# Kernel tuning notes

Hardware: AMD Instinct MI355X
Metric: run time of the kernel (lower is better)

## Reference

```python
import jax, jax.numpy as jnp
import numpy as np

B, T, C = 2, 2048, 1024
H = 16
D = C // H  # head_dim = 64


def setup_inputs() -> dict:
    key = jax.random.key(0)
    k1, k2, k3 = jax.random.split(key, 3)
    x = jax.random.normal(k1, (B, T, C), dtype=jnp.float32)
    # causal mask: True means 'mask out' (masked_fill semantics)
    attn_mask = jnp.triu(jnp.ones((T, T), dtype=bool), k=1)[None, None]
    W_attn = jax.random.normal(k2, (C, 3 * C), dtype=jnp.float32) * (1.0 / np.sqrt(C))
    b_attn = jnp.zeros((3 * C,), dtype=jnp.float32)
    W_proj = jax.random.normal(k3, (C, C), dtype=jnp.float32) * (1.0 / np.sqrt(C))
    b_proj = jnp.zeros((C,), dtype=jnp.float32)
    return {"x": x, "attn_mask": attn_mask, "W_attn": W_attn, "b_attn": b_attn,
            "W_proj": W_proj, "b_proj": b_proj}


def reference(x, attn_mask, W_attn, b_attn, W_proj, b_proj):
    Bb, Tt, Cc = x.shape
    qkv = x @ W_attn + b_attn                      # [B,T,3C]
    q, k, v = jnp.split(qkv, 3, axis=-1)
    def to_heads(t):
        return t.reshape(Bb, Tt, H, D).transpose(0, 2, 1, 3)  # [B,H,T,D]
    q, k, v = to_heads(q), to_heads(k), to_heads(v)
    scale = 1.0 / np.sqrt(D).astype(np.float32)
    attn = jnp.einsum('bhqd,bhkd->bhqk', q, k) * scale  # [B,H,T,T]
    attn = jnp.where(attn_mask, -jnp.inf, attn)
    attn = jax.nn.softmax(attn, axis=-1)
    y = jnp.einsum('bhqk,bhkd->bhqd', attn, v)          # [B,H,T,D]
    y = y.transpose(0, 2, 1, 3).reshape(Bb, Tt, Cc)
    return y @ W_proj + b_proj
```

## Files before the change

kernel.cpp:

```cpp
#include <hip/hip_runtime.h>
#include <math.h>


#define TSEQ 2048
#define NHD  16
#define DH   64
#define CDIM 1024

typedef __attribute__((ext_vector_type(8))) short bf16x8;
typedef __attribute__((ext_vector_type(4))) float f32x4;

#define MFMA(a, b, c) __builtin_amdgcn_mfma_f32_16x16x32_bf16((a), (b), (c), 0, 0, 0)

__device__ __forceinline__ ushort f2bf(float f) {
    unsigned u = __builtin_bit_cast(unsigned, f);
    u += 0x7FFFu + ((u >> 16) & 1u);
    return (ushort)(u >> 16);
}
__device__ __forceinline__ float bf2f(ushort h) {
    unsigned u = ((unsigned)h) << 16;
    return __builtin_bit_cast(float, u);
}

__global__ __launch_bounds__(256) void cast_k(const float* __restrict__ in,
                                              ushort* __restrict__ out, int n4) {
    int i = blockIdx.x * 256 + threadIdx.x;
    const int stride = gridDim.x * 256;
    for (; i < n4; i += stride) {
        float4 f = ((const float4*)in)[i];
        ushort4 o;
        o.x = f2bf(f.x); o.y = f2bf(f.y); o.z = f2bf(f.z); o.w = f2bf(f.w);
        ((ushort4*)out)[i] = o;
    }
}

__global__ __launch_bounds__(256) void transpose_k(const float* __restrict__ in,
                                                   ushort* __restrict__ out,
                                                   int R, int C) {
    __shared__ float t[32][33];
    const int tx = threadIdx.x, ty = threadIdx.y;
    const int c0 = blockIdx.x * 32, r0 = blockIdx.y * 32;
#pragma unroll
    for (int i = 0; i < 4; ++i)
        t[ty + i * 8][tx] = in[(size_t)(r0 + ty + i * 8) * C + c0 + tx];
    __syncthreads();
#pragma unroll
    for (int i = 0; i < 4; ++i)
        out[(size_t)(c0 + ty + i * 8) * R + r0 + tx] = f2bf(t[tx][ty + i * 8]);
}

__global__ __launch_bounds__(256) void qkv_k(const ushort* __restrict__ X,
                                             const ushort* __restrict__ Wt,
                                             const float* __restrict__ bias,
                                             ushort* __restrict__ qb,
                                             ushort* __restrict__ kb,
                                             ushort* __restrict__ vtb) {
    const int fid = blockIdx.x;
    const int nf = (fid & 7) * 96 + (fid >> 3);
    const int mt = nf / 24, nt = nf % 24;
    const int m0 = mt * 128, n0 = nt * 128;
    const int tid = threadIdx.x, lane = tid & 63, w = tid >> 6;
    const int l15 = lane & 15, g = lane >> 4;
    const int wm = w >> 1, wn = w & 1;

    const ushort* Ar[4]; const ushort* Br[4];
#pragma unroll
    for (int s = 0; s < 4; ++s) {
        Ar[s] = X  + (size_t)(m0 + wm * 64 + s * 16 + l15) * 1024 + g * 8;
        Br[s] = Wt + (size_t)(n0 + wn * 64 + s * 16 + l15) * 1024 + g * 8;
    }
    f32x4 acc[4][4] = {};
    bf16x8 a[4], b[4], a2[4], b2[4];
#pragma unroll
    for (int s = 0; s < 4; ++s) { a[s] = *(const bf16x8*)(Ar[s]); b[s] = *(const bf16x8*)(Br[s]); }

    for (int kk = 0; kk < 1024; kk += 32) {
        if (kk + 32 < 1024) {
#pragma unroll
            for (int s = 0; s < 4; ++s) {
                a2[s] = *(const bf16x8*)(Ar[s] + kk + 32);
                b2[s] = *(const bf16x8*)(Br[s] + kk + 32);
            }
        }
#pragma unroll
        for (int i = 0; i < 4; ++i)
#pragma unroll
            for (int j = 0; j < 4; ++j)
                acc[i][j] = MFMA(a[i], b[j], acc[i][j]);
#pragma unroll
        for (int s = 0; s < 4; ++s) { a[s] = a2[s]; b[s] = b2[s]; }
    }
#pragma unroll
    for (int j = 0; j < 4; ++j) {
        const int n = n0 + wn * 64 + j * 16 + l15;
        const float bv = bias[n];
        const int which = n >> 10;
        const int c = n & 1023, h = c >> 6, d = c & 63;
#pragma unroll
        for (int i = 0; i < 4; ++i)
#pragma unroll
            for (int r = 0; r < 4; ++r) {
                const int m = m0 + wm * 64 + i * 16 + g * 4 + r;
                const int bb = m >> 11, t = m & 2047;
                const float val = acc[i][j][r] + bv;
                const int bh = bb * NHD + h;
                if (which == 0)
                    qb[((size_t)bh * TSEQ + t) * 64 + d] = f2bf(val * 0.125f);
                else if (which == 1)
                    kb[((size_t)bh * TSEQ + t) * 64 + d] = f2bf(val);
                else
                    vtb[((size_t)bh * 64 + d) * TSEQ + t] = f2bf(val);
            }
    }
}

__global__ __launch_bounds__(256, 4) void attn_k(const ushort* __restrict__ Q,
                                                 const ushort* __restrict__ K,
                                                 const ushort* __restrict__ VT,
                                                 ushort* __restrict__ Yh,
                                                 ushort* __restrict__ Yl) {
    __shared__ ushort P[4][16][72];
    __shared__ float Om[4][16][66];
    __shared__ float Mw[4][16];
    __shared__ float Lw[4][16];

    const int fid = blockIdx.x;
    const int nf = (fid & 7) * 512 + (fid >> 3);
    const int bh = nf >> 7, q16 = nf & 127;
    const int tid = threadIdx.x, w = tid >> 6, lane = tid & 63;
    const int l15 = lane & 15, g = lane >> 4;
    const int q0 = q16 * 16;

    const ushort* Qb = Q  + (size_t)bh * TSEQ * 64;
    const ushort* Kb = K  + (size_t)bh * TSEQ * 64;
    const ushort* Vb = VT + (size_t)bh * 64 * TSEQ;

    bf16x8 qf0 = *(const bf16x8*)(Qb + (size_t)(q0 + l15) * 64 + g * 8);
    bf16x8 qf1 = *(const bf16x8*)(Qb + (size_t)(q0 + l15) * 64 + 32 + g * 8);

    f32x4 o[4] = {};
    float m_run = -INFINITY, l_run = 0.f;
    const int nT = q0 / 64 + 1;

    for (int t = w; t < nT; t += 4) {
        const int kv0 = t * 64;
        bf16x8 ak[4][2];
#pragma unroll
        for (int s = 0; s < 4; ++s) {
            const ushort* kr = Kb + (size_t)(kv0 + s * 16 + l15) * 64 + g * 8;
            ak[s][0] = *(const bf16x8*)(kr);
            ak[s][1] = *(const bf16x8*)(kr + 32);
        }
        f32x4 s4[4] = {};
#pragma unroll
        for (int s = 0; s < 4; ++s) {
            s4[s] = MFMA(ak[s][0], qf0, s4[s]);
            s4[s] = MFMA(ak[s][1], qf1, s4[s]);
        }
        bf16x8 av[4][2];
#pragma unroll
        for (int s = 0; s < 4; ++s) {
            const ushort* vr = Vb + (size_t)(s * 16 + l15) * TSEQ + kv0 + g * 8;
            av[s][0] = *(const bf16x8*)(vr);
            av[s][1] = *(const bf16x8*)(vr + 32);
        }
        if (kv0 + 63 > q0) {
#pragma unroll
            for (int s = 0; s < 4; ++s)
#pragma unroll
                for (int r = 0; r < 4; ++r) {
                    const int kg = kv0 + s * 16 + g * 4 + r;
                    if (kg > q0 + l15) s4[s][r] = -INFINITY;
                }
        }
        float mx = -INFINITY;
#pragma unroll
        for (int s = 0; s < 4; ++s)
#pragma unroll
            for (int r = 0; r < 4; ++r) mx = fmaxf(mx, s4[s][r]);
        mx = fmaxf(mx, __shfl_xor(mx, 16));
        mx = fmaxf(mx, __shfl_xor(mx, 32));
        const float mnew = fmaxf(m_run, mx);
        const float alpha = __expf(m_run - mnew);
        float lsum = 0.f;
#pragma unroll
        for (int s = 0; s < 4; ++s) {
            float p0 = __expf(s4[s][0] - mnew);
            float p1 = __expf(s4[s][1] - mnew);
            float p2 = __expf(s4[s][2] - mnew);
            float p3 = __expf(s4[s][3] - mnew);
            lsum += (p0 + p1) + (p2 + p3);
            ushort4 pw;
            pw.x = f2bf(p0); pw.y = f2bf(p1); pw.z = f2bf(p2); pw.w = f2bf(p3);
            *(ushort4*)&P[w][l15][s * 16 + g * 4] = pw;
        }
        lsum += __shfl_xor(lsum, 16);
        lsum += __shfl_xor(lsum, 32);
        l_run = l_run * alpha + lsum;
        m_run = mnew;
#pragma unroll
        for (int s = 0; s < 4; ++s)
#pragma unroll
            for (int r = 0; r < 4; ++r) o[s][r] *= alpha;
        bf16x8 pb0 = *(const bf16x8*)&P[w][l15][g * 8];
        bf16x8 pb1 = *(const bf16x8*)&P[w][l15][32 + g * 8];
#pragma unroll
        for (int s = 0; s < 4; ++s) {
            o[s] = MFMA(av[s][0], pb0, o[s]);
            o[s] = MFMA(av[s][1], pb1, o[s]);
        }
    }

    if (g == 0) { Mw[w][l15] = m_run; Lw[w][l15] = l_run; }
#pragma unroll
    for (int s = 0; s < 4; ++s) {
        *(float2*)&Om[w][l15][s * 16 + g * 4]     = make_float2(o[s][0], o[s][1]);
        *(float2*)&Om[w][l15][s * 16 + g * 4 + 2] = make_float2(o[s][2], o[s][3]);
    }
    __syncthreads();

    const float m0v = Mw[0][l15], m1v = Mw[1][l15], m2v = Mw[2][l15], m3v = Mw[3][l15];
    const float m_tot = fmaxf(fmaxf(m0v, m1v), fmaxf(m2v, m3v));
    float l_tot = 0.f;
    f32x4 od = {};
#pragma unroll
    for (int j = 0; j < 4; ++j) {
        const float sc = __expf(Mw[j][l15] - m_tot);
        l_tot += Lw[j][l15] * sc;
        const float2 p0 = *(const float2*)&Om[j][l15][w * 16 + g * 4];
        const float2 p1 = *(const float2*)&Om[j][l15][w * 16 + g * 4 + 2];
        od[0] += p0.x * sc; od[1] += p0.y * sc;
        od[2] += p1.x * sc; od[3] += p1.y * sc;
    }
    const float inv = 1.f / l_tot;
    const int trow = q0 + l15;
    const size_t base = ((size_t)(bh >> 4) * TSEQ + trow) * CDIM + (bh & 15) * 64
                        + w * 16 + g * 4;
    ushort4 hv, lv;
    float v;
    v = od[0] * inv; hv.x = f2bf(v); lv.x = f2bf(v - bf2f(hv.x));
    v = od[1] * inv; hv.y = f2bf(v); lv.y = f2bf(v - bf2f(hv.y));
    v = od[2] * inv; hv.z = f2bf(v); lv.z = f2bf(v - bf2f(hv.z));
    v = od[3] * inv; hv.w = f2bf(v); lv.w = f2bf(v - bf2f(hv.w));
    *(ushort4*)&Yh[base] = hv;
    *(ushort4*)&Yl[base] = lv;
}

__global__ __launch_bounds__(256, 3) void proj_k(const ushort* __restrict__ Yh,
                                                 const ushort* __restrict__ Yl,
                                                 const ushort* __restrict__ Wt,
                                                 const float* __restrict__ bias,
                                                 float* __restrict__ out) {
    __shared__ float S[64][68];
    const int fid = blockIdx.x;
    const int nf = (fid & 7) * 128 + (fid >> 3);
    const int mt = nf >> 4, nt = nf & 15;
    const int m0 = mt * 64, n0 = nt * 64;
    const int tid = threadIdx.x, w = tid >> 6, lane = tid & 63;
    const int l15 = lane & 15, g = lane >> 4;
    const int k0 = w * 256;

    const ushort* Ah[4]; const ushort* Al[4]; const ushort* Br[4];
#pragma unroll
    for (int s = 0; s < 4; ++s) {
        const size_t arow = (size_t)(m0 + s * 16 + l15) * 1024 + k0 + g * 8;
        Ah[s] = Yh + arow;
        Al[s] = Yl + arow;
        Br[s] = Wt + (size_t)(n0 + s * 16 + l15) * 1024 + k0 + g * 8;
    }
    f32x4 acc[4][4] = {};
#pragma unroll 2
    for (int kk = 0; kk < 256; kk += 32) {
        bf16x8 ah[4], al[4], b[4];
#pragma unroll
        for (int s = 0; s < 4; ++s) {
            ah[s] = *(const bf16x8*)(Ah[s] + kk);
            al[s] = *(const bf16x8*)(Al[s] + kk);
            b[s]  = *(const bf16x8*)(Br[s] + kk);
        }
#pragma unroll
        for (int i = 0; i < 4; ++i)
#pragma unroll
            for (int j = 0; j < 4; ++j) {
                acc[i][j] = MFMA(ah[i], b[j], acc[i][j]);
                acc[i][j] = MFMA(al[i], b[j], acc[i][j]);
            }
    }
    for (int ww = 0; ww < 4; ++ww) {
        if (ww == w) {
#pragma unroll
            for (int i = 0; i < 4; ++i)
#pragma unroll
                for (int j = 0; j < 4; ++j) {
                    f32x4* dst = (f32x4*)&S[j * 16 + l15][i * 16 + g * 4];
                    if (ww == 0) *dst = acc[i][j];
                    else         *dst = *dst + acc[i][j];
                }
        }
        __syncthreads();
    }
    const int m = tid >> 2;
    const int nq = (tid & 3) * 16;
    float* orow = out + (size_t)(m0 + m) * 1024 + n0 + nq;
#pragma unroll
    for (int u = 0; u < 16; u += 4) {
        const float4 bv = *(const float4*)&bias[n0 + nq + u];
        float4 vo;
        vo.x = S[nq + u + 0][m] + bv.x;
        vo.y = S[nq + u + 1][m] + bv.y;
        vo.z = S[nq + u + 2][m] + bv.z;
        vo.w = S[nq + u + 3][m] + bv.w;
        *(float4*)&orow[u] = vo;
    }
}

extern "C" void kernel_launch(void* const* d_in, const int* in_sizes, int n_in,
                              void* d_out, int out_size, void* d_ws, size_t ws_size,
                              hipStream_t stream) {
    (void)in_sizes; (void)n_in; (void)out_size; (void)ws_size;
    const float* x      = (const float*)d_in[0];
    const float* W_attn = (const float*)d_in[2];
    const float* b_attn = (const float*)d_in[3];
    const float* W_proj = (const float*)d_in[4];
    const float* b_proj = (const float*)d_in[5];
    float* out = (float*)d_out;

    ushort* xb  = (ushort*)d_ws;
    ushort* wta = xb  + 4194304;
    ushort* wtp = wta + 3145728;
    ushort* qb  = wtp + 1048576;
    ushort* kb  = qb  + 4194304;
    ushort* vtb = kb  + 4194304;
    ushort* yh  = vtb + 4194304;
    ushort* yl  = yh  + 4194304;

    cast_k<<<1024, 256, 0, stream>>>(x, xb, 4194304 / 4);
    transpose_k<<<dim3(96, 32), dim3(32, 8), 0, stream>>>(W_attn, wta, 1024, 3072);
    transpose_k<<<dim3(32, 32), dim3(32, 8), 0, stream>>>(W_proj, wtp, 1024, 1024);
    qkv_k<<<768, 256, 0, stream>>>(xb, wta, b_attn, qb, kb, vtb);
    attn_k<<<4096, 256, 0, stream>>>(qb, kb, vtb, yh, yl);
    proj_k<<<1024, 256, 0, stream>>>(yh, yl, wtp, b_proj, out);
}
```

Baseline: 389.8 us.

## Process 32 query rows per attention block to reuse K/V loads

Each attention block now handles two 16-row query sub-tiles (32 rows) instead of one, so every K and V fragment loaded from global memory feeds MFMAs for both sub-tiles. The grid shrinks from 4096 to 2048 blocks. The goal is to halve K/V global traffic per query row and raise MFMA work per load. In exchange, register pressure roughly doubles for accumulators and scores, which may hurt occupancy under launch_bounds(256,4). Causal load balance across waves also gets coarser, and the final cross-wave merge now runs twice with an extra barrier.

```diff
diff --git a/kernel.cpp b/kernel.cpp
--- a/kernel.cpp
+++ b/kernel.cpp
@@ -119,43 +119,56 @@
                                                  const ushort* __restrict__ VT,
                                                  ushort* __restrict__ Yh,
                                                  ushort* __restrict__ Yl) {
-    __shared__ ushort P[4][16][72];
+    __shared__ ushort P[4][2][16][72];
     __shared__ float Om[4][16][66];
-    __shared__ float Mw[4][16];
-    __shared__ float Lw[4][16];
+    __shared__ float Mw[4][2][16];
+    __shared__ float Lw[4][2][16];
 
     const int fid = blockIdx.x;
-    const int nf = (fid & 7) * 512 + (fid >> 3);
-    const int bh = nf >> 7, q16 = nf & 127;
+    const int nf = (fid & 7) * 256 + (fid >> 3);
+    const int bh = nf >> 6, q32 = nf & 63;
     const int tid = threadIdx.x, w = tid >> 6, lane = tid & 63;
     const int l15 = lane & 15, g = lane >> 4;
-    const int q0 = q16 * 16;
+    const int q0 = q32 * 32;
 
     const ushort* Qb = Q  + (size_t)bh * TSEQ * 64;
     const ushort* Kb = K  + (size_t)bh * TSEQ * 64;
     const ushort* Vb = VT + (size_t)bh * 64 * TSEQ;
 
-    bf16x8 qf0 = *(const bf16x8*)(Qb + (size_t)(q0 + l15) * 64 + g * 8);
-    bf16x8 qf1 = *(const bf16x8*)(Qb + (size_t)(q0 + l15) * 64 + 32 + g * 8);
-
-    f32x4 o[4] = {};
-    float m_run = -INFINITY, l_run = 0.f;
+    bf16x8 qf[2][2];
+#pragma unroll
+    for (int u = 0; u < 2; ++u) {
+        const ushort* qr = Qb + (size_t)(q0 + u * 16 + l15) * 64 + g * 8;
+        qf[u][0] = *(const bf16x8*)(qr);
+        qf[u][1] = *(const bf16x8*)(qr + 32);
+    }
+
+    f32x4 o[2][4] = {};
+    float m_run[2] = {-INFINITY, -INFINITY};
+    float l_run[2] = {0.f, 0.f};
     const int nT = q0 / 64 + 1;
 
     for (int t = w; t < nT; t += 4) {
         const int kv0 = t * 64;
-        bf16x8 ak[4][2];
-#pragma unroll
-        for (int s = 0; s < 4; ++s) {
-            const ushort* kr = Kb + (size_t)(kv0 + s * 16 + l15) * 64 + g * 8;
-            ak[s][0] = *(const bf16x8*)(kr);
-            ak[s][1] = *(const bf16x8*)(kr + 32);
-        }
-        f32x4 s4[4] = {};
-#pragma unroll
-        for (int s = 0; s < 4; ++s) {
-            s4[s] = MFMA(ak[s][0], qf0, s4[s]);
-            s4[s] = MFMA(ak[s][1], qf1, s4[s]);
+        f32x4 s4[2][4] = {};
+#pragma unroll
+        for (int h = 0; h < 2; ++h) {
+            bf16x8 ak[2][2];
+#pragma unroll
+            for (int ss = 0; ss < 2; ++ss) {
+                const int s = h * 2 + ss;
+                const ushort* kr = Kb + (size_t)(kv0 + s * 16 + l15) * 64 + g * 8;
+                ak[ss][0] = *(const bf16x8*)(kr);
+                ak[ss][1] = *(const bf16x8*)(kr + 32);
+            }
+#pragma unroll
+            for (int u = 0; u < 2; ++u)
+#pragma unroll
+                for (int ss = 0; ss < 2; ++ss) {
+                    const int s = h * 2 + ss;
+                    s4[u][s] = MFMA(ak[ss][0], qf[u][0], s4[u][s]);
+                    s4[u][s] = MFMA(ak[ss][1], qf[u][1], s4[u][s]);
+                }
         }
         bf16x8 av[4][2];
 #pragma unroll
@@ -166,84 +179,113 @@
         }
         if (kv0 + 63 > q0) {
 #pragma unroll
+            for (int u = 0; u < 2; ++u)
+#pragma unroll
+                for (int s = 0; s < 4; ++s)
+#pragma unroll
+                    for (int r = 0; r < 4; ++r) {
+                        const int kg = kv0 + s * 16 + g * 4 + r;
+                        if (kg > q0 + u * 16 + l15) s4[u][s][r] = -INFINITY;
+                    }
+        }
+        float mx[2];
+#pragma unroll
+        for (int u = 0; u < 2; ++u) {
+            mx[u] = -INFINITY;
+#pragma unroll
             for (int s = 0; s < 4; ++s)
 #pragma unroll
-                for (int r = 0; r < 4; ++r) {
-                    const int kg = kv0 + s * 16 + g * 4 + r;
-                    if (kg > q0 + l15) s4[s][r] = -INFINITY;
-                }
-        }
-        float mx = -INFINITY;
-#pragma unroll
-        for (int s = 0; s < 4; ++s)
-#pragma unroll
-            for (int r = 0; r < 4; ++r) mx = fmaxf(mx, s4[s][r]);
-        mx = fmaxf(mx, __shfl_xor(mx, 16));
-        mx = fmaxf(mx, __shfl_xor(mx, 32));
-        const float mnew = fmaxf(m_run, mx);
-        const float alpha = __expf(m_run - mnew);
-        float lsum = 0.f;
+                for (int r = 0; r < 4; ++r) mx[u] = fmaxf(mx[u], s4[u][s][r]);
+        }
+        mx[0] = fmaxf(mx[0], __shfl_xor(mx[0], 16));
+        mx[1] = fmaxf(mx[1], __shfl_xor(mx[1], 16));
+        mx[0] = fmaxf(mx[0], __shfl_xor(mx[0], 32));
+        mx[1] = fmaxf(mx[1], __shfl_xor(mx[1], 32));
+        float lsum[2], alpha[2];
+#pragma unroll
+        for (int u = 0; u < 2; ++u) {
+            const float mnew = fmaxf(m_run[u], mx[u]);
+            alpha[u] = __expf(m_run[u] - mnew);
+            lsum[u] = 0.f;
+#pragma unroll
+            for (int s = 0; s < 4; ++s) {
+                float p0 = __expf(s4[u][s][0] - mnew);
+                float p1 = __expf(s4[u][s][1] - mnew);
+                float p2 = __expf(s4[u][s][2] - mnew);
+                float p3 = __expf(s4[u][s][3] - mnew);
+                lsum[u] += (p0 + p1) + (p2 + p3);
+                ushort4 pw;
+                pw.x = f2bf(p0); pw.y = f2bf(p1); pw.z = f2bf(p2); pw.w = f2bf(p3);
+                *(ushort4*)&P[w][u][l15][s * 16 + g * 4] = pw;
+            }
+            m_run[u] = mnew;
+        }
+        lsum[0] += __shfl_xor(lsum[0], 16);
+        lsum[1] += __shfl_xor(lsum[1], 16);
+        lsum[0] += __shfl_xor(lsum[0], 32);
+        lsum[1] += __shfl_xor(lsum[1], 32);
+#pragma unroll
+        for (int u = 0; u < 2; ++u) {
+            l_run[u] = l_run[u] * alpha[u] + lsum[u];
+#pragma unroll
+            for (int s = 0; s < 4; ++s)
+#pragma unroll
+                for (int r = 0; r < 4; ++r) o[u][s][r] *= alpha[u];
+        }
+        bf16x8 pb[2][2];
+#pragma unroll
+        for (int u = 0; u < 2; ++u) {
+            pb[u][0] = *(const bf16x8*)&P[w][u][l15][g * 8];
+            pb[u][1] = *(const bf16x8*)&P[w][u][l15][32 + g * 8];
+        }
+#pragma unroll
+        for (int u = 0; u < 2; ++u)
+#pragma unroll
+            for (int s = 0; s < 4; ++s) {
+                o[u][s] = MFMA(av[s][0], pb[u][0], o[u][s]);
+                o[u][s] = MFMA(av[s][1], pb[u][1], o[u][s]);
+            }
+    }
+
+    if (g == 0) {
+        Mw[w][0][l15] = m_run[0]; Mw[w][1][l15] = m_run[1];
+        Lw[w][0][l15] = l_run[0]; Lw[w][1][l15] = l_run[1];
+    }
+#pragma unroll
+    for (int u = 0; u < 2; ++u) {
+        if (u) __syncthreads();
 #pragma unroll
         for (int s = 0; s < 4; ++s) {
-            float p0 = __expf(s4[s][0] - mnew);
-            float p1 = __expf(s4[s][1] - mnew);
-            float p2 = __expf(s4[s][2] - mnew);
-            float p3 = __expf(s4[s][3] - mnew);
-            lsum += (p0 + p1) + (p2 + p3);
-            ushort4 pw;
-            pw.x = f2bf(p0); pw.y = f2bf(p1); pw.z = f2bf(p2); pw.w = f2bf(p3);
-            *(ushort4*)&P[w][l15][s * 16 + g * 4] = pw;
-        }
-        lsum += __shfl_xor(lsum, 16);
-        lsum += __shfl_xor(lsum, 32);
-        l_run = l_run * alpha + lsum;
-        m_run = mnew;
-#pragma unroll
-        for (int s = 0; s < 4; ++s)
-#pragma unroll
-            for (int r = 0; r < 4; ++r) o[s][r] *= alpha;
-        bf16x8 pb0 = *(const bf16x8*)&P[w][l15][g * 8];
-        bf16x8 pb1 = *(const bf16x8*)&P[w][l15][32 + g * 8];
-#pragma unroll
-        for (int s = 0; s < 4; ++s) {
-            o[s] = MFMA(av[s][0], pb0, o[s]);
-            o[s] = MFMA(av[s][1], pb1, o[s]);
-        }
-    }
-
-    if (g == 0) { Mw[w][l15] = m_run; Lw[w][l15] = l_run; }
-#pragma unroll
-    for (int s = 0; s < 4; ++s) {
-        *(float2*)&Om[w][l15][s * 16 + g * 4]     = make_float2(o[s][0], o[s][1]);
-        *(float2*)&Om[w][l15][s * 16 + g * 4 + 2] = make_float2(o[s][2], o[s][3]);
-    }
-    __syncthreads();
-
-    const float m0v = Mw[0][l15], m1v = Mw[1][l15], m2v = Mw[2][l15], m3v = Mw[3][l15];
-    const float m_tot = fmaxf(fmaxf(m0v, m1v), fmaxf(m2v, m3v));
-    float l_tot = 0.f;
-    f32x4 od = {};
-#pragma unroll
-    for (int j = 0; j < 4; ++j) {
-        const float sc = __expf(Mw[j][l15] - m_tot);
-        l_tot += Lw[j][l15] * sc;
-        const float2 p0 = *(const float2*)&Om[j][l15][w * 16 + g * 4];
-        const float2 p1 = *(const float2*)&Om[j][l15][w * 16 + g * 4 + 2];
-        od[0] += p0.x * sc; od[1] += p0.y * sc;
-        od[2] += p1.x * sc; od[3] += p1.y * sc;
-    }
-    const float inv = 1.f / l_tot;
-    const int trow = q0 + l15;
-    const size_t base = ((size_t)(bh >> 4) * TSEQ + trow) * CDIM + (bh & 15) * 64
-                        + w * 16 + g * 4;
-    ushort4 hv, lv;
-    float v;
-    v = od[0] * inv; hv.x = f2bf(v); lv.x = f2bf(v - bf2f(hv.x));
-    v = od[1] * inv; hv.y = f2bf(v); lv.y = f2bf(v - bf2f(hv.y));
-    v = od[2] * inv; hv.z = f2bf(v); lv.z = f2bf(v - bf2f(hv.z));
-    v = od[3] * inv; hv.w = f2bf(v); lv.w = f2bf(v - bf2f(hv.w));
-    *(ushort4*)&Yh[base] = hv;
-    *(ushort4*)&Yl[base] = lv;
+            *(float2*)&Om[w][l15][s * 16 + g * 4]     = make_float2(o[u][s][0], o[u][s][1]);
+            *(float2*)&Om[w][l15][s * 16 + g * 4 + 2] = make_float2(o[u][s][2], o[u][s][3]);
+        }
+        __syncthreads();
+        const float m_tot = fmaxf(fmaxf(Mw[0][u][l15], Mw[1][u][l15]),
+                                  fmaxf(Mw[2][u][l15], Mw[3][u][l15]));
+        float l_tot = 0.f;
+        f32x4 od = {};
+#pragma unroll
+        for (int j = 0; j < 4; ++j) {
+            const float sc = __expf(Mw[j][u][l15] - m_tot);
+            l_tot += Lw[j][u][l15] * sc;
+            const float2 p0 = *(const float2*)&Om[j][l15][w * 16 + g * 4];
+            const float2 p1 = *(const float2*)&Om[j][l15][w * 16 + g * 4 + 2];
+            od[0] += p0.x * sc; od[1] += p0.y * sc;
+            od[2] += p1.x * sc; od[3] += p1.y * sc;
+        }
+        const float inv = 1.f / l_tot;
+        const int trow = q0 + u * 16 + l15;
+        const size_t base = ((size_t)(bh >> 4) * TSEQ + trow) * CDIM
+                            + (bh & 15) * 64 + w * 16 + g * 4;
+        ushort4 hv, lv;
+        float v;
+        v = od[0] * inv; hv.x = f2bf(v); lv.x = f2bf(v - bf2f(hv.x));
+        v = od[1] * inv; hv.y = f2bf(v); lv.y = f2bf(v - bf2f(hv.y));
+        v = od[2] * inv; hv.z = f2bf(v); lv.z = f2bf(v - bf2f(hv.z));
+        v = od[3] * inv; hv.w = f2bf(v); lv.w = f2bf(v - bf2f(hv.w));
+        *(ushort4*)&Yh[base] = hv;
+        *(ushort4*)&Yl[base] = lv;
+    }
 }
 
 __global__ __launch_bounds__(256, 3) void proj_k(const ushort* __restrict__ Yh,
@@ -338,6 +380,6 @@
     transpose_k<<<dim3(96, 32), dim3(32, 8), 0, stream>>>(W_attn, wta, 1024, 3072);
     transpose_k<<<dim3(32, 32), dim3(32, 8), 0, stream>>>(W_proj, wtp, 1024, 1024);
     qkv_k<<<768, 256, 0, stream>>>(xb, wta, b_attn, qb, kb, vtb);
-    attn_k<<<4096, 256, 0, stream>>>(qb, kb, vtb, yh, yl);
+    attn_k<<<2048, 256, 0, stream>>>(qb, kb, vtb, yh, yl);
     proj_k<<<1024, 256, 0, stream>>>(yh, yl, wtp, b_proj, out);
 }
```

Result: slower. 411.1 us (+5.5%).

## Stage QKV GEMM tiles through swizzled LDS with register prefetch

Applied to the files above, without the earlier changes.

The QKV projection GEMM now loads 128x64 tiles of X and Wt cooperatively into shared memory, using an XOR swizzle to avoid bank conflicts. Before, each wave read its operands straight from global memory, so tiles were fetched redundantly across waves. Register double-buffering prefetches the next K-slab while MFMAs run on the current one, and launch bounds request 3 blocks per CU. The cost is two barriers per K step and higher LDS and register pressure.

```diff
diff --git a/kernel.cpp b/kernel.cpp
--- a/kernel.cpp
+++ b/kernel.cpp
@@ -49,12 +49,15 @@
         out[(size_t)(c0 + ty + i * 8) * R + r0 + tx] = f2bf(t[tx][ty + i * 8]);
 }
 
-__global__ __launch_bounds__(256) void qkv_k(const ushort* __restrict__ X,
-                                             const ushort* __restrict__ Wt,
-                                             const float* __restrict__ bias,
-                                             ushort* __restrict__ qb,
-                                             ushort* __restrict__ kb,
-                                             ushort* __restrict__ vtb) {
+__global__ __launch_bounds__(256, 3) void qkv_k(const ushort* __restrict__ X,
+                                                const ushort* __restrict__ Wt,
+                                                const float* __restrict__ bias,
+                                                ushort* __restrict__ qb,
+                                                ushort* __restrict__ kb,
+                                                ushort* __restrict__ vtb) {
+    __shared__ ushort Al[128][64];
+    __shared__ ushort Bl[128][64];
+
     const int fid = blockIdx.x;
     const int nf = (fid & 7) * 96 + (fid >> 3);
     const int mt = nf / 24, nt = nf % 24;
@@ -63,32 +66,55 @@
     const int l15 = lane & 15, g = lane >> 4;
     const int wm = w >> 1, wn = w & 1;
 
-    const ushort* Ar[4]; const ushort* Br[4];
-#pragma unroll
-    for (int s = 0; s < 4; ++s) {
-        Ar[s] = X  + (size_t)(m0 + wm * 64 + s * 16 + l15) * 1024 + g * 8;
-        Br[s] = Wt + (size_t)(n0 + wn * 64 + s * 16 + l15) * 1024 + g * 8;
-    }
+    int srow[4], sch[4];
+#pragma unroll
+    for (int i = 0; i < 4; ++i) {
+        const int c = tid + 256 * i;
+        srow[i] = c >> 3;
+        sch[i] = c & 7;
+    }
+
+    bf16x8 ra[4], rb[4];
+#pragma unroll
+    for (int i = 0; i < 4; ++i) {
+        ra[i] = *(const bf16x8*)&X [(size_t)(m0 + srow[i]) * 1024 + sch[i] * 8];
+        rb[i] = *(const bf16x8*)&Wt[(size_t)(n0 + srow[i]) * 1024 + sch[i] * 8];
+    }
+
     f32x4 acc[4][4] = {};
-    bf16x8 a[4], b[4], a2[4], b2[4];
-#pragma unroll
-    for (int s = 0; s < 4; ++s) { a[s] = *(const bf16x8*)(Ar[s]); b[s] = *(const bf16x8*)(Br[s]); }
-
-    for (int kk = 0; kk < 1024; kk += 32) {
-        if (kk + 32 < 1024) {
+
+    for (int k0 = 0; k0 < 1024; k0 += 64) {
+        __syncthreads();
+#pragma unroll
+        for (int i = 0; i < 4; ++i) {
+            const int sc = (sch[i] ^ (srow[i] & 7)) * 8;
+            *(bf16x8*)&Al[srow[i]][sc] = ra[i];
+            *(bf16x8*)&Bl[srow[i]][sc] = rb[i];
+        }
+        __syncthreads();
+        if (k0 + 64 < 1024) {
+#pragma unroll
+            for (int i = 0; i < 4; ++i) {
+                ra[i] = *(const bf16x8*)&X [(size_t)(m0 + srow[i]) * 1024 + k0 + 64 + sch[i] * 8];
+                rb[i] = *(const bf16x8*)&Wt[(size_t)(n0 + srow[i]) * 1024 + k0 + 64 + sch[i] * 8];
+            }
+        }
+#pragma unroll
+        for (int kk = 0; kk < 2; ++kk) {
+            bf16x8 af[4], bf[4];
 #pragma unroll
             for (int s = 0; s < 4; ++s) {
-                a2[s] = *(const bf16x8*)(Ar[s] + kk + 32);
-                b2[s] = *(const bf16x8*)(Br[s] + kk + 32);
+                const int arow = wm * 64 + s * 16 + l15;
+                af[s] = *(const bf16x8*)&Al[arow][((kk * 4 + g) ^ (arow & 7)) * 8];
+                const int brow = wn * 64 + s * 16 + l15;
+                bf[s] = *(const bf16x8*)&Bl[brow][((kk * 4 + g) ^ (brow & 7)) * 8];
             }
-        }
-#pragma unroll
-        for (int i = 0; i < 4; ++i)
-#pragma unroll
-            for (int j = 0; j < 4; ++j)
-                acc[i][j] = MFMA(a[i], b[j], acc[i][j]);
-#pragma unroll
-        for (int s = 0; s < 4; ++s) { a[s] = a2[s]; b[s] = b2[s]; }
+#pragma unroll
+            for (int i = 0; i < 4; ++i)
+#pragma unroll
+                for (int j = 0; j < 4; ++j)
+                    acc[i][j] = MFMA(af[i], bf[j], acc[i][j]);
+        }
     }
 #pragma unroll
     for (int j = 0; j < 4; ++j) {
```

After: 329.1 us. 15.6% less time.
